# Performance work log

Hardware: AMD Instinct MI355X
Metric: run time of the kernel (lower is better)

The kernel has to match this reference:

```python
import jax, jax.numpy as jnp
import numpy as np

EMBED = 1024
HEADS = 16
HEAD_DIM = EMBED // HEADS


def setup_inputs() -> dict:
    key = jax.random.key(0)
    ks = jax.random.split(key, 6)
    B, T, C = 4, 2048, EMBED
    x = jax.random.normal(ks[0], (B, T, C), dtype=jnp.float32)
    # random binary mask [B,1,1,T]; keep at least one valid key per row by forcing first position to 1
    mask = jax.random.randint(ks[1], (B, 1, 1, T), 0, 2, dtype=jnp.int32)
    mask = mask.at[..., 0].set(1)
    scale = 1.0 / np.sqrt(C)
    qkv_w = jax.random.normal(ks[2], (3 * C, C), dtype=jnp.float32) * scale  # torch Linear weight [out,in]
    qkv_b = jax.random.normal(ks[3], (3 * C,), dtype=jnp.float32) * scale
    out_w = jax.random.normal(ks[4], (C, C), dtype=jnp.float32) * scale
    out_b = jax.random.normal(ks[5], (C,), dtype=jnp.float32) * scale
    return {"x": x, "mask": mask, "qkv_w": qkv_w, "qkv_b": qkv_b, "out_w": out_w, "out_b": out_b}


def reference(x, mask, qkv_w, qkv_b, out_w, out_b):
    B, T, C = x.shape
    H, D = HEADS, HEAD_DIM
    qkv = x @ qkv_w.T + qkv_b  # [B,T,3C]
    qkv = qkv.reshape(B, T, 3, H, D).transpose(2, 0, 3, 1, 4)  # [3,B,H,T,D]
    q, k, v = qkv[0], qkv[1], qkv[2]
    scores = jnp.einsum('bhqd,bhkd->bhqk', q, k) / np.sqrt(D)
    scores = jnp.where(mask == 0, -jnp.inf, scores)
    attn = jax.nn.softmax(scores, axis=-1)
    out = jnp.einsum('bhqk,bhkd->bhqd', attn, v)
    out = out.transpose(0, 2, 1, 3).reshape(B, T, C)
    return out @ out_w.T + out_b
```

## Files before the change

### kernel.cpp

```cpp
#include <hip/hip_runtime.h>
#include <hip/hip_bf16.h>

typedef _Float16 f16;
typedef _Float16 f16x4_t __attribute__((ext_vector_type(4)));
typedef _Float16 f16x8 __attribute__((ext_vector_type(8)));
typedef float f32x4 __attribute__((ext_vector_type(4)));

#define AS1(p) ((const __attribute__((address_space(1))) void*)(p))
#define AS3(p) ((__attribute__((address_space(3))) void*)(p))

__device__ __forceinline__ void gload_lds16(const f16* g, f16* l) {
    __builtin_amdgcn_global_load_lds(AS1(g), AS3(l), 16, 0, 0);
}

__device__ __forceinline__ f16x8 cvt8(float4 u, float4 v) {
    f16x8 r;
    r[0] = (f16)u.x; r[1] = (f16)u.y; r[2] = (f16)u.z; r[3] = (f16)u.w;
    r[4] = (f16)v.x; r[5] = (f16)v.y; r[6] = (f16)v.z; r[7] = (f16)v.w;
    return r;
}

#define Q_SCALE 0.180336880111f

__global__ __launch_bounds__(256) void cvt_f32_f16(
    const float* __restrict__ src, f16* __restrict__ dst, int n8)
{
    int idx = blockIdx.x * 256 + threadIdx.x;
    int stride = gridDim.x * 256;
    for (int i = idx; i < n8; i += stride) {
        size_t o = (size_t)i * 8;
        float4 u = *(const float4*)&src[o];
        float4 v = *(const float4*)&src[o + 4];
        *(f16x8*)&dst[o] = cvt8(u, v);
    }
}

__global__ __launch_bounds__(64) void scan_mask(
    const int* __restrict__ mask, int* __restrict__ cpos, int* __restrict__ nkv)
{
    const int b = blockIdx.x;
    const int lane = threadIdx.x;
    const int* mb = mask + b * 2048;
    int run = 0;
    for (int c = 0; c < 2048; c += 64) {
        int v = (mb[c + lane] != 0) ? 1 : 0;
        unsigned long long bits = __ballot(v);
        int pre = __popcll(bits & ((1ull << lane) - 1ull));
        cpos[b * 2048 + c + lane] = v ? (run + pre) : -1;
        run += __popcll(bits);
    }
    if (lane == 0) nkv[b] = run;
}

__global__ __launch_bounds__(256) void fill_tail(
    const int* __restrict__ nkv, f16* __restrict__ k_c, f16* __restrict__ vt_c)
{
    const int b = blockIdx.x, h = blockIdx.y;
    const int run = nkv[b];
    const int pad = (run + 63) & ~63;
    const int tail = pad - run;
    if (tail == 0) return;
    const int tid = threadIdx.x;
    const size_t bh = (size_t)(b * 16 + h);
    f16x8 z = {};
    f16* kp = k_c + bh * (size_t)(2048 * 64) + (size_t)run * 64;
    const int kn = tail * 64;
    for (int x = tid * 8; x < kn; x += 256 * 8)
        *(f16x8*)&kp[x] = z;
    const int wave = tid >> 6, lane = tid & 63;
    for (int d = wave; d < 64; d += 4) {
        f16* vp = vt_c + (bh * 64 + d) * 2048 + run;
        if (lane < tail) vp[lane] = (f16)0.f;
    }
}

__global__ __launch_bounds__(256) void gemm_qkv_f16(
    const f16* __restrict__ A16, const f16* __restrict__ Bw16,
    const float* __restrict__ bias, const int* __restrict__ cpos,
    f16* __restrict__ q_g, f16* __restrict__ k_g, f16* __restrict__ vt_g,
    int M, int K)
{
    constexpr int BK = 64;
    __shared__ f16 As[128 * BK], Bs[128 * BK];

    const int tid  = threadIdx.x;
    const int lane = tid & 63, wave = tid >> 6;
    const int wy = wave >> 1, wx = wave & 1;
    const int lrow = lane & 15, quad = lane >> 4;
    const size_t m0 = (size_t)blockIdx.y * 128;
    const size_t n0 = (size_t)blockIdx.x * 128;
    const int srow = lane >> 3;
    const int sgrp = lane & 7;
    const int x0 = ((quad)     ^ (lrow & 7)) * 8;
    const int x1 = ((4 + quad) ^ (lrow & 7)) * 8;

    f32x4 acc[4][4] = {};

    for (int k0 = 0; k0 < K; k0 += BK) {
        __syncthreads();
#pragma unroll
        for (int j = 0; j < 4; ++j) {
            int rg  = wave * 4 + j;
            int row = rg * 8 + srow;
            int grp = sgrp ^ srow;
            gload_lds16(&A16[(m0 + row) * (size_t)K + k0 + grp * 8],
                        &As[rg * 512 + lane * 8]);
            gload_lds16(&Bw16[(n0 + row) * (size_t)K + k0 + grp * 8],
                        &Bs[rg * 512 + lane * 8]);
        }
        __syncthreads();

        f16x8 a0[4], a1[4], b0[4], b1[4];
#pragma unroll
        for (int i = 0; i < 4; ++i) {
            const int r = (wy * 64 + i * 16 + lrow) * BK;
            a0[i] = *(const f16x8*)&As[r + x0];
            a1[i] = *(const f16x8*)&As[r + x1];
        }
#pragma unroll
        for (int j = 0; j < 4; ++j) {
            const int r = (wx * 64 + j * 16 + lrow) * BK;
            b0[j] = *(const f16x8*)&Bs[r + x0];
            b1[j] = *(const f16x8*)&Bs[r + x1];
        }
#pragma unroll
        for (int i = 0; i < 4; ++i)
#pragma unroll
            for (int j = 0; j < 4; ++j) {
                acc[i][j] = __builtin_amdgcn_mfma_f32_16x16x32_f16(a0[i], b0[j], acc[i][j], 0, 0, 0);
                acc[i][j] = __builtin_amdgcn_mfma_f32_16x16x32_f16(a1[i], b1[j], acc[i][j], 0, 0, 0);
            }
    }

    const int region = (int)(n0 >> 10);
#pragma unroll
    for (int i = 0; i < 4; ++i) {
        size_t row = m0 + wy * 64 + i * 16 + quad * 4;
        int b = (int)(row >> 11);
        int t = (int)(row & 2047);
        int cp[4];
        if (region != 0) {
            int4 c4 = *(const int4*)&cpos[b * 2048 + t];
            cp[0] = c4.x; cp[1] = c4.y; cp[2] = c4.z; cp[3] = c4.w;
        }
#pragma unroll
        for (int j = 0; j < 4; ++j) {
            int col = (int)n0 + wx * 64 + j * 16 + lrow;
            float bb = bias[col];
            int cl = col & 1023, hh = cl >> 6, d = cl & 63;
            if (region == 0) {
                size_t o = ((size_t)(b * 16 + hh) * 2048 + t) * 64 + d;
#pragma unroll
                for (int r = 0; r < 4; ++r)
                    q_g[o + (size_t)r * 64] = (f16)((acc[i][j][r] + bb) * Q_SCALE);
            } else if (region == 1) {
#pragma unroll
                for (int r = 0; r < 4; ++r)
                    if (cp[r] >= 0)
                        k_g[((size_t)(b * 16 + hh) * 2048 + cp[r]) * 64 + d] =
                            (f16)(acc[i][j][r] + bb);
            } else {
#pragma unroll
                for (int r = 0; r < 4; ++r)
                    if (cp[r] >= 0)
                        vt_g[((size_t)(b * 16 + hh) * 64 + d) * 2048 + cp[r]] =
                            (f16)(acc[i][j][r] + bb);
            }
        }
    }
}

__global__ __launch_bounds__(256) void gemm2_f16(
    const f16* __restrict__ A16, const f16* __restrict__ Bw16,
    const float* __restrict__ bias, float* __restrict__ C,
    int M, int N, int K)
{
    constexpr int BK = 64;
    __shared__ f16 As[128 * BK], Bs[128 * BK];

    const int tid  = threadIdx.x;
    const int lane = tid & 63, wave = tid >> 6;
    const int wy = wave >> 1, wx = wave & 1;
    const int lrow = lane & 15, quad = lane >> 4;
    const size_t m0 = (size_t)blockIdx.y * 128;
    const size_t n0 = (size_t)blockIdx.x * 128;
    const int srow = lane >> 3, sgrp = lane & 7;
    const int x0 = ((quad)     ^ (lrow & 7)) * 8;
    const int x1 = ((4 + quad) ^ (lrow & 7)) * 8;

    f32x4 acc[4][4] = {};

    for (int k0 = 0; k0 < K; k0 += BK) {
        __syncthreads();
#pragma unroll
        for (int j = 0; j < 4; ++j) {
            int rg  = wave * 4 + j;
            int row = rg * 8 + srow;
            int grp = sgrp ^ srow;
            gload_lds16(&A16[(m0 + row) * (size_t)K + k0 + grp * 8],
                        &As[rg * 512 + lane * 8]);
            gload_lds16(&Bw16[(n0 + row) * (size_t)K + k0 + grp * 8],
                        &Bs[rg * 512 + lane * 8]);
        }
        __syncthreads();

        f16x8 a0[4], a1[4], b0[4], b1[4];
#pragma unroll
        for (int i = 0; i < 4; ++i) {
            const int r = (wy * 64 + i * 16 + lrow) * BK;
            a0[i] = *(const f16x8*)&As[r + x0];
            a1[i] = *(const f16x8*)&As[r + x1];
        }
#pragma unroll
        for (int j = 0; j < 4; ++j) {
            const int r = (wx * 64 + j * 16 + lrow) * BK;
            b0[j] = *(const f16x8*)&Bs[r + x0];
            b1[j] = *(const f16x8*)&Bs[r + x1];
        }
#pragma unroll
        for (int i = 0; i < 4; ++i)
#pragma unroll
            for (int j = 0; j < 4; ++j) {
                acc[i][j] = __builtin_amdgcn_mfma_f32_16x16x32_f16(a0[i], b0[j], acc[i][j], 0, 0, 0);
                acc[i][j] = __builtin_amdgcn_mfma_f32_16x16x32_f16(a1[i], b1[j], acc[i][j], 0, 0, 0);
            }
    }

#pragma unroll
    for (int i = 0; i < 4; ++i) {
        size_t row = m0 + wy * 64 + i * 16 + quad * 4;
#pragma unroll
        for (int j = 0; j < 4; ++j) {
            size_t col = n0 + wx * 64 + j * 16 + lrow;
            float bb = bias[col];
#pragma unroll
            for (int r = 0; r < 4; ++r)
                C[(row + r) * N + col] = acc[i][j][r] + bb;
        }
    }
}

__global__ __launch_bounds__(256) void attn_f16(
    const f16* __restrict__ q_g, const f16* __restrict__ k_g,
    const f16* __restrict__ vt_g, const int* __restrict__ nkv,
    f16* __restrict__ att, int B, int T)
{
    constexpr int LDP = 72;
    __shared__ f16 Ks_s[2][64 * 64];
    __shared__ f16 Vt_s[2][64 * 64];
    __shared__ f16 Pt[128 * LDP];

    const int tid  = threadIdx.x;
    const int lane = tid & 63, wave = tid >> 6;
    const int lrow = lane & 15, quad = lane >> 4;
    const int bid = ((int)blockIdx.x & 7) * 128 + ((int)blockIdx.x >> 3);
    const int qt = bid & 15;
    const int h  = (bid >> 4) & 15;
    const int b  = bid >> 8;
    const size_t base = (size_t)b * T;
    const size_t bh = (size_t)(b * 16 + h);
    const f16* qg_base = q_g  + bh * (2048 * 64);
    const f16* kg_base = k_g  + bh * (2048 * 64);
    const f16* vt_base = vt_g + bh * (64 * 2048);

    const int nk = nkv[b];
    const int ntiles = (nk + 63) >> 6;

    const int x0 = ((quad)     ^ (lrow & 7)) * 8;
    const int x1 = ((4 + quad) ^ (lrow & 7)) * 8;

    f16x8 aq[2][2];
#pragma unroll
    for (int qi = 0; qi < 2; ++qi)
#pragma unroll
        for (int ks = 0; ks < 2; ++ks)
            aq[qi][ks] = *(const f16x8*)&qg_base[
                (size_t)(qt * 128 + wave * 32 + qi * 16 + lrow) * 64 + ks * 32 + quad * 8];

    f32x4 oacc[2][4] = {};
    float l_part[2] = {0.f, 0.f};

    const int srow0 = (lane >> 3);
    const int sgrp  = (lane & 7);

    auto stage = [&](int kt, int bsel) {
        const f16* kT = kg_base + kt * 4096;
#pragma unroll
        for (int j = 0; j < 2; ++j) {
            int rg  = wave + j * 4;
            int row = rg * 8 + srow0;
            int grp = sgrp ^ (row & 7);
            gload_lds16(&kT[row * 64 + grp * 8], &Ks_s[bsel][rg * 512 + lane * 8]);
            gload_lds16(&vt_base[(size_t)row * 2048 + kt * 64 + grp * 8],
                        &Vt_s[bsel][rg * 512 + lane * 8]);
        }
    };

    stage(0, 0);
    __syncthreads();

    for (int kt = 0; kt < ntiles; ++kt) {
        const int cur = kt & 1;
        if (kt + 1 < ntiles) stage(kt + 1, cur ^ 1);

        const f16* Ks = Ks_s[cur];
        const f16* Vt = Vt_s[cur];

        f32x4 s[2][4];
        __builtin_amdgcn_s_setprio(1);
#pragma unroll
        for (int ni = 0; ni < 4; ++ni) {
            const int key = ni * 16 + lrow;
            f16x8 k0 = *(const f16x8*)&Ks[key * 64 + x0];
            f16x8 k1 = *(const f16x8*)&Ks[key * 64 + x1];
#pragma unroll
            for (int qi = 0; qi < 2; ++qi) {
                f32x4 t = {0.f, 0.f, 0.f, 0.f};
                t = __builtin_amdgcn_mfma_f32_16x16x32_f16(k0, aq[qi][0], t, 0, 0, 0);
                t = __builtin_amdgcn_mfma_f32_16x16x32_f16(k1, aq[qi][1], t, 0, 0, 0);
                s[qi][ni] = t;
            }
        }
        __builtin_amdgcn_s_setprio(0);

        const int rem = nk - kt * 64;
        auto softmax = [&](bool masked) {
#pragma unroll
            for (int qi = 0; qi < 2; ++qi)
#pragma unroll
                for (int ni = 0; ni < 4; ++ni) {
                    float p[4];
#pragma unroll
                    for (int r = 0; r < 4; ++r) {
                        float e = __builtin_amdgcn_exp2f(s[qi][ni][r]);
                        p[r] = (!masked || (ni * 16 + quad * 4 + r) < rem) ? e : 0.f;
                    }
                    l_part[qi] += (p[0] + p[1]) + (p[2] + p[3]);
                    f16x4_t pk;
#pragma unroll
                    for (int r = 0; r < 4; ++r) pk[r] = (f16)p[r];
                    *(f16x4_t*)&Pt[(wave * 32 + qi * 16 + lrow) * LDP + ni * 16 + quad * 4] = pk;
                }
        };
        if (rem >= 64) softmax(false); else softmax(true);

        f16x8 pf[2][2];
#pragma unroll
        for (int qi = 0; qi < 2; ++qi)
#pragma unroll
            for (int ks = 0; ks < 2; ++ks)
                pf[qi][ks] = *(const f16x8*)&Pt[(wave * 32 + qi * 16 + lrow) * LDP + ks * 32 + quad * 8];
        __builtin_amdgcn_s_setprio(1);
#pragma unroll
        for (int di = 0; di < 4; ++di) {
            const int d = di * 16 + lrow;
            f16x8 v0 = *(const f16x8*)&Vt[d * 64 + x0];
            f16x8 v1 = *(const f16x8*)&Vt[d * 64 + x1];
#pragma unroll
            for (int qi = 0; qi < 2; ++qi) {
                oacc[qi][di] = __builtin_amdgcn_mfma_f32_16x16x32_f16(v0, pf[qi][0], oacc[qi][di], 0, 0, 0);
                oacc[qi][di] = __builtin_amdgcn_mfma_f32_16x16x32_f16(v1, pf[qi][1], oacc[qi][di], 0, 0, 0);
            }
        }
        __builtin_amdgcn_s_setprio(0);

        __syncthreads();
    }

#pragma unroll
    for (int qi = 0; qi < 2; ++qi) {
        float v = l_part[qi];
        v += __shfl_xor(v, 16);
        v += __shfl_xor(v, 32);
        float inv = 1.f / v;
        int q = qt * 128 + wave * 32 + qi * 16 + lrow;
#pragma unroll
        for (int di = 0; di < 4; ++di) {
            f16x4_t o;
#pragma unroll
            for (int r = 0; r < 4; ++r) o[r] = (f16)(oacc[qi][di][r] * inv);
            *(f16x4_t*)&att[(base + q) * 1024 + h * 64 + di * 16 + quad * 4] = o;
        }
    }
}

extern "C" void kernel_launch(void* const* d_in, const int* in_sizes, int n_in,
                              void* d_out, int out_size, void* d_ws, size_t ws_size,
                              hipStream_t stream) {
    const float* x     = (const float*)d_in[0];
    const int*   mask  = (const int*)d_in[1];
    const float* qkv_w = (const float*)d_in[2];
    const float* qkv_b = (const float*)d_in[3];
    const float* out_w = (const float*)d_in[4];
    const float* out_b = (const float*)d_in[5];
    float* out = (float*)d_out;

    const int B = 4, T = 2048;
    const int M = B * T;
    char* ws = (char*)d_ws;
    f16* q_g = (f16*)(ws);
    f16* k_g = (f16*)(ws + 16777216);
    f16* vt  = (f16*)(ws + 33554432);
    f16* att = (f16*)(ws + 50331648);

    f16* x16 = (f16*)d_out;
    f16* w16 = (f16*)((char*)d_out + 16777216);
    int* cpos = (int*)((char*)d_out + 23068672);
    int* nkv  = cpos + 4 * 2048;
    f16* ow16 = q_g;

    dim3 blk(256);
    cvt_f32_f16<<<dim3(2048), blk, 0, stream>>>(x, x16, M * 1024 / 8);
    cvt_f32_f16<<<dim3(1024), blk, 0, stream>>>(qkv_w, w16, 3072 * 1024 / 8);
    scan_mask<<<dim3(4), dim3(64), 0, stream>>>(mask, cpos, nkv);
    fill_tail<<<dim3(4, 16), blk, 0, stream>>>(nkv, k_g, vt);
    gemm_qkv_f16<<<dim3(3072 / 128, M / 128), blk, 0, stream>>>(x16, w16, qkv_b, cpos, q_g, k_g, vt, M, 1024);
    attn_f16<<<dim3(B * 16 * 16), blk, 0, stream>>>(q_g, k_g, vt, nkv, att, B, T);
    cvt_f32_f16<<<dim3(512), blk, 0, stream>>>(out_w, ow16, 1024 * 1024 / 8);
    gemm2_f16<<<dim3(1024 / 128, M / 128), blk, 0, stream>>>(att, ow16, out_b, out, M, 1024, 1024);
}
```

Baseline: 279.5 us.

## Compute K/V projections only for unmasked tokens via gather; fuse preprocessing kernels

The mask scan now emits a gather list of valid token indices, and the QKV GEMM is split so K/V tiles gather only valid rows of x and skip tiles past the valid count. This removes projection work on masked keys (about half the tokens) and the scattered per-element K/Vt stores. The fill_tail kernel is dropped, V stores become vectorised, and the x/weight conversions plus the mask scan are fused into one launch. Risk: padded rows use token 0 rather than zeros, so the attention kernel must still mask keys beyond nkv.

```diff
diff --git a/kernel.cpp b/kernel.cpp
--- a/kernel.cpp
+++ b/kernel.cpp
@@ -21,6 +21,43 @@
 }
 
 #define Q_SCALE 0.180336880111f
+
+__global__ __launch_bounds__(256) void pre_pass(
+    const float* __restrict__ x, const float* __restrict__ qw,
+    const int* __restrict__ mask, f16* __restrict__ x16,
+    f16* __restrict__ w16, int* __restrict__ gpos, int* __restrict__ nkv)
+{
+    const int blk = blockIdx.x;
+    if (blk >= 2048) {
+        const int b = blk - 2048;
+        if (threadIdx.x < 64) {
+            const int lane = threadIdx.x;
+            const int* mb = mask + b * 2048;
+            int run = 0;
+            for (int c = 0; c < 2048; c += 64) {
+                int v = (mb[c + lane] != 0) ? 1 : 0;
+                unsigned long long bits = __ballot(v);
+                int pre = __popcll(bits & ((1ull << lane) - 1ull));
+                if (v) gpos[b * 2048 + run + pre] = c + lane;
+                run += __popcll(bits);
+            }
+            if (lane == 0) nkv[b] = run;
+        }
+        return;
+    }
+    const int nx8 = 8192 * 1024 / 8;
+    const int nw8 = 3072 * 1024 / 8;
+    int idx = blk * 256 + threadIdx.x;
+    const int stride = 2048 * 256;
+    for (int i = idx; i < nx8 + nw8; i += stride) {
+        const float* s; f16* d;
+        if (i < nx8) { size_t o = (size_t)i * 8;          s = x  + o; d = x16 + o; }
+        else         { size_t o = (size_t)(i - nx8) * 8;  s = qw + o; d = w16 + o; }
+        float4 u = *(const float4*)s;
+        float4 v = *(const float4*)(s + 4);
+        *(f16x8*)d = cvt8(u, v);
+    }
+}
 
 __global__ __launch_bounds__(256) void cvt_f32_f16(
     const float* __restrict__ src, f16* __restrict__ dst, int n8)
@@ -35,78 +72,63 @@
     }
 }
 
-__global__ __launch_bounds__(64) void scan_mask(
-    const int* __restrict__ mask, int* __restrict__ cpos, int* __restrict__ nkv)
+__global__ __launch_bounds__(256) void gemm_qkv_f16(
+    const f16* __restrict__ x16, const f16* __restrict__ w16,
+    const float* __restrict__ bias, const int* __restrict__ gpos,
+    const int* __restrict__ nkv, f16* __restrict__ q_g,
+    f16* __restrict__ k_g, f16* __restrict__ vt_g)
 {
-    const int b = blockIdx.x;
-    const int lane = threadIdx.x;
-    const int* mb = mask + b * 2048;
-    int run = 0;
-    for (int c = 0; c < 2048; c += 64) {
-        int v = (mb[c + lane] != 0) ? 1 : 0;
-        unsigned long long bits = __ballot(v);
-        int pre = __popcll(bits & ((1ull << lane) - 1ull));
-        cpos[b * 2048 + c + lane] = v ? (run + pre) : -1;
-        run += __popcll(bits);
-    }
-    if (lane == 0) nkv[b] = run;
-}
-
-__global__ __launch_bounds__(256) void fill_tail(
-    const int* __restrict__ nkv, f16* __restrict__ k_c, f16* __restrict__ vt_c)
-{
-    const int b = blockIdx.x, h = blockIdx.y;
-    const int run = nkv[b];
-    const int pad = (run + 63) & ~63;
-    const int tail = pad - run;
-    if (tail == 0) return;
-    const int tid = threadIdx.x;
-    const size_t bh = (size_t)(b * 16 + h);
-    f16x8 z = {};
-    f16* kp = k_c + bh * (size_t)(2048 * 64) + (size_t)run * 64;
-    const int kn = tail * 64;
-    for (int x = tid * 8; x < kn; x += 256 * 8)
-        *(f16x8*)&kp[x] = z;
-    const int wave = tid >> 6, lane = tid & 63;
-    for (int d = wave; d < 64; d += 4) {
-        f16* vp = vt_c + (bh * 64 + d) * 2048 + run;
-        if (lane < tail) vp[lane] = (f16)0.f;
-    }
-}
-
-__global__ __launch_bounds__(256) void gemm_qkv_f16(
-    const f16* __restrict__ A16, const f16* __restrict__ Bw16,
-    const float* __restrict__ bias, const int* __restrict__ cpos,
-    f16* __restrict__ q_g, f16* __restrict__ k_g, f16* __restrict__ vt_g,
-    int M, int K)
-{
-    constexpr int BK = 64;
+    constexpr int BK = 64, K = 1024;
     __shared__ f16 As[128 * BK], Bs[128 * BK];
 
     const int tid  = threadIdx.x;
     const int lane = tid & 63, wave = tid >> 6;
     const int wy = wave >> 1, wx = wave & 1;
     const int lrow = lane & 15, quad = lane >> 4;
-    const size_t m0 = (size_t)blockIdx.y * 128;
-    const size_t n0 = (size_t)blockIdx.x * 128;
     const int srow = lane >> 3;
     const int sgrp = lane & 7;
     const int x0 = ((quad)     ^ (lrow & 7)) * 8;
     const int x1 = ((4 + quad) ^ (lrow & 7)) * 8;
 
+    const int z  = blockIdx.z;
+    const int bx = blockIdx.x, by = blockIdx.y;
+    int b_kv = 0, mt = 0, nk = 0, nbase, n0;
+    if (z == 0) {
+        if (bx >= 8) return;
+        nbase = 0; n0 = bx * 128;
+    } else {
+        b_kv = by >> 4; mt = by & 15;
+        nk = nkv[b_kv];
+        if (mt * 128 >= nk) return;
+        nbase = 1024; n0 = bx * 128;
+    }
+
+    const f16* arow[4];
+    const f16* brow[4];
+#pragma unroll
+    for (int j = 0; j < 4; ++j) {
+        int rit = (wave * 4 + j) * 8 + srow;
+        int trow;
+        if (z == 0) {
+            trow = by * 128 + rit;
+        } else {
+            int ct = mt * 128 + rit;
+            int t = (ct < nk) ? gpos[b_kv * 2048 + ct] : 0;
+            trow = b_kv * 2048 + t;
+        }
+        arow[j] = x16 + (size_t)trow * K + (sgrp ^ srow) * 8;
+        brow[j] = w16 + (size_t)(nbase + n0 + rit) * K + (sgrp ^ srow) * 8;
+    }
+
     f32x4 acc[4][4] = {};
 
     for (int k0 = 0; k0 < K; k0 += BK) {
         __syncthreads();
 #pragma unroll
         for (int j = 0; j < 4; ++j) {
-            int rg  = wave * 4 + j;
-            int row = rg * 8 + srow;
-            int grp = sgrp ^ srow;
-            gload_lds16(&A16[(m0 + row) * (size_t)K + k0 + grp * 8],
-                        &As[rg * 512 + lane * 8]);
-            gload_lds16(&Bw16[(n0 + row) * (size_t)K + k0 + grp * 8],
-                        &Bs[rg * 512 + lane * 8]);
+            int rg = wave * 4 + j;
+            gload_lds16(arow[j] + k0, &As[rg * 512 + lane * 8]);
+            gload_lds16(brow[j] + k0, &Bs[rg * 512 + lane * 8]);
         }
         __syncthreads();
 
@@ -132,39 +154,44 @@
             }
     }
 
-    const int region = (int)(n0 >> 10);
-#pragma unroll
-    for (int i = 0; i < 4; ++i) {
-        size_t row = m0 + wy * 64 + i * 16 + quad * 4;
-        int b = (int)(row >> 11);
-        int t = (int)(row & 2047);
-        int cp[4];
-        if (region != 0) {
-            int4 c4 = *(const int4*)&cpos[b * 2048 + t];
-            cp[0] = c4.x; cp[1] = c4.y; cp[2] = c4.z; cp[3] = c4.w;
-        }
-#pragma unroll
-        for (int j = 0; j < 4; ++j) {
-            int col = (int)n0 + wx * 64 + j * 16 + lrow;
-            float bb = bias[col];
-            int cl = col & 1023, hh = cl >> 6, d = cl & 63;
-            if (region == 0) {
+    if (z == 0) {
+#pragma unroll
+        for (int i = 0; i < 4; ++i) {
+            size_t row = (size_t)by * 128 + wy * 64 + i * 16 + quad * 4;
+            int b = (int)(row >> 11);
+            int t = (int)(row & 2047);
+#pragma unroll
+            for (int j = 0; j < 4; ++j) {
+                int col = n0 + wx * 64 + j * 16 + lrow;
+                float bb = bias[col];
+                int hh = col >> 6, d = col & 63;
                 size_t o = ((size_t)(b * 16 + hh) * 2048 + t) * 64 + d;
 #pragma unroll
                 for (int r = 0; r < 4; ++r)
                     q_g[o + (size_t)r * 64] = (f16)((acc[i][j][r] + bb) * Q_SCALE);
-            } else if (region == 1) {
-#pragma unroll
-                for (int r = 0; r < 4; ++r)
-                    if (cp[r] >= 0)
-                        k_g[((size_t)(b * 16 + hh) * 2048 + cp[r]) * 64 + d] =
-                            (f16)(acc[i][j][r] + bb);
-            } else {
-#pragma unroll
-                for (int r = 0; r < 4; ++r)
-                    if (cp[r] >= 0)
-                        vt_g[((size_t)(b * 16 + hh) * 64 + d) * 2048 + cp[r]] =
-                            (f16)(acc[i][j][r] + bb);
+            }
+        }
+    } else {
+        const int region = n0 >> 10;
+#pragma unroll
+        for (int i = 0; i < 4; ++i) {
+            int ct = mt * 128 + wy * 64 + i * 16 + quad * 4;
+#pragma unroll
+            for (int j = 0; j < 4; ++j) {
+                int col = n0 + wx * 64 + j * 16 + lrow;
+                float bb = bias[1024 + col];
+                int cl = col & 1023, hh = cl >> 6, d = cl & 63;
+                size_t bh = (size_t)(b_kv * 16 + hh);
+                if (region == 0) {
+#pragma unroll
+                    for (int r = 0; r < 4; ++r)
+                        k_g[(bh * 2048 + ct + r) * 64 + d] = (f16)(acc[i][j][r] + bb);
+                } else {
+                    f16x4_t pv;
+#pragma unroll
+                    for (int r = 0; r < 4; ++r) pv[r] = (f16)(acc[i][j][r] + bb);
+                    *(f16x4_t*)&vt_g[(bh * 64 + d) * 2048 + ct] = pv;
+                }
             }
         }
     }
@@ -405,16 +432,13 @@
 
     f16* x16 = (f16*)d_out;
     f16* w16 = (f16*)((char*)d_out + 16777216);
-    int* cpos = (int*)((char*)d_out + 23068672);
-    int* nkv  = cpos + 4 * 2048;
+    int* gpos = (int*)((char*)d_out + 23068672);
+    int* nkv  = gpos + 4 * 2048;
     f16* ow16 = q_g;
 
     dim3 blk(256);
-    cvt_f32_f16<<<dim3(2048), blk, 0, stream>>>(x, x16, M * 1024 / 8);
-    cvt_f32_f16<<<dim3(1024), blk, 0, stream>>>(qkv_w, w16, 3072 * 1024 / 8);
-    scan_mask<<<dim3(4), dim3(64), 0, stream>>>(mask, cpos, nkv);
-    fill_tail<<<dim3(4, 16), blk, 0, stream>>>(nkv, k_g, vt);
-    gemm_qkv_f16<<<dim3(3072 / 128, M / 128), blk, 0, stream>>>(x16, w16, qkv_b, cpos, q_g, k_g, vt, M, 1024);
+    pre_pass<<<dim3(2052), blk, 0, stream>>>(x, qkv_w, mask, x16, w16, gpos, nkv);
+    gemm_qkv_f16<<<dim3(16, 64, 2), blk, 0, stream>>>(x16, w16, qkv_b, gpos, nkv, q_g, k_g, vt);
     attn_f16<<<dim3(B * 16 * 16), blk, 0, stream>>>(q_g, k_g, vt, nkv, att, B, T);
     cvt_f32_f16<<<dim3(512), blk, 0, stream>>>(out_w, ow16, 1024 * 1024 / 8);
     gemm2_f16<<<dim3(1024 / 128, M / 128), blk, 0, stream>>>(att, ow16, out_b, out, M, 1024, 1024);
```

New measurement: 272.4 us. -2.5%, faster.
